# Kernel tuning notes

Hardware: AMD Instinct MI355X
Metric: run time of the kernel (lower is better)

The kernel has to match this reference:

```python
import jax, jax.numpy as jnp
import numpy as np

EMBED_DIM = 768
NUM_HEADS = 12
HEAD_DIM = EMBED_DIM // NUM_HEADS
LN_EPS = 1e-5


def setup_inputs() -> dict:
    key = jax.random.key(0)
    ks = jax.random.split(key, 10)
    D = EMBED_DIM
    s = 1.0 / np.sqrt(D)
    x = jax.random.normal(ks[0], (2, 4096, D), dtype=jnp.float32)
    # nn.Linear weights stored as [out, in]; we keep [in, out] for x @ W.
    Wq = jax.random.uniform(ks[1], (D, D), jnp.float32, -s, s)
    bq = jax.random.uniform(ks[2], (D,), jnp.float32, -s, s)
    Wk = jax.random.uniform(ks[3], (D, D), jnp.float32, -s, s)
    bk = jax.random.uniform(ks[4], (D,), jnp.float32, -s, s)
    Wv = jax.random.uniform(ks[5], (D, D), jnp.float32, -s, s)
    bv = jax.random.uniform(ks[6], (D,), jnp.float32, -s, s)
    Wo = jax.random.uniform(ks[7], (D, D), jnp.float32, -s, s)
    bo = jax.random.uniform(ks[8], (D,), jnp.float32, -s, s)
    ln_g = jnp.ones((D,), jnp.float32)
    ln_b = jnp.zeros((D,), jnp.float32)
    return {"x": x, "Wq": Wq, "bq": bq, "Wk": Wk, "bk": bk,
            "Wv": Wv, "bv": bv, "Wo": Wo, "bo": bo,
            "ln_g": ln_g, "ln_b": ln_b}


def layer_norm(x, g, b):
    mu = jnp.mean(x, axis=-1, keepdims=True)
    var = jnp.mean(jnp.square(x - mu), axis=-1, keepdims=True)
    return (x - mu) * jax.lax.rsqrt(var + LN_EPS) * g + b


def reference(x, Wq, bq, Wk, bk, Wv, bv, Wo, bo, ln_g, ln_b):
    B, S, D = x.shape
    H, Hd = NUM_HEADS, HEAD_DIM
    residual = x
    xn = layer_norm(x, ln_g, ln_b)
    # [B,S,D] -> [B,H,S,Hd]
    def heads(t):
        return t.reshape(B, S, H, Hd).transpose(0, 2, 1, 3)
    q = heads(xn @ Wq + bq)
    k = heads(xn @ Wk + bk)
    v = heads(xn @ Wv + bv)
    scores = jnp.einsum('bhqd,bhkd->bhqk', q, k) / np.sqrt(Hd).astype(np.float32)
    attn = jax.nn.softmax(scores, axis=-1)  # dropout is identity in eval
    out = jnp.einsum('bhqk,bhkd->bhqd', attn, v)
    out = out.transpose(0, 2, 1, 3).reshape(B, S, D)
    out = out @ Wo + bo
    return out + residual
```

## Files before the change

### kernel.cpp

```cpp
#include <hip/hip_runtime.h>
#include <hip/hip_bf16.h>
#include <math.h>

constexpr int Bz = 2, Sq = 4096, Dm = 768, Hn = 12, Hd = 64;
constexpr int Mrows = Bz * Sq;
constexpr int LDQKV = 2304;

typedef short bf16x8 __attribute__((ext_vector_type(8)));
typedef float f32x4 __attribute__((ext_vector_type(4)));

__device__ __forceinline__ short f2bf(float f) {
  unsigned u = __builtin_bit_cast(unsigned, f);
  u += 0x7fffu + ((u >> 16) & 1u);
  return (short)(u >> 16);
}

__device__ __forceinline__ unsigned cvt_pk_bf16(float a, float b) {
  unsigned r;
  asm("v_cvt_pk_bf16_f32 %0, %1, %2" : "=v"(r) : "v"(a), "v"(b));
  return r;
}

__global__ __launch_bounds__(256) void wprep_kernel(
    const float* __restrict__ Wq, const float* __restrict__ Wk,
    const float* __restrict__ Wv, const float* __restrict__ Wo,
    short* __restrict__ Wt) {
  __shared__ short T[64][72];
  const float* W = blockIdx.z == 0 ? Wq : blockIdx.z == 1 ? Wk
                 : blockIdx.z == 2 ? Wv : Wo;
  const int k0 = blockIdx.x * 64, n0 = blockIdx.y * 64;
  const int t = threadIdx.x;
  const int c4 = (t & 15) * 4, r = t >> 4;
#pragma unroll
  for (int i = 0; i < 4; ++i) {
    const int k = r + i * 16;
    const float4 wv = *(const float4*)(W + (size_t)(k0 + k) * 768 + n0 + c4);
    T[c4 + 0][k] = f2bf(wv.x);
    T[c4 + 1][k] = f2bf(wv.y);
    T[c4 + 2][k] = f2bf(wv.z);
    T[c4 + 3][k] = f2bf(wv.w);
  }
  __syncthreads();
  const int cn = t & 7, nn = t >> 3;
#pragma unroll
  for (int i = 0; i < 2; ++i) {
    const int n = nn + i * 32;
    *(bf16x8*)(Wt + ((size_t)blockIdx.z * 768 + n0 + n) * 768 + k0 + cn * 8) =
        *(const bf16x8*)&T[n][cn * 8];
  }
}

__global__ __launch_bounds__(256) void biaspack_kernel(
    const float* __restrict__ bq, const float* __restrict__ bk,
    const float* __restrict__ bv, const float* __restrict__ bo,
    float* __restrict__ dst) {
  const int j = blockIdx.x * 256 + threadIdx.x;
  dst[j] = j < 768 ? bq[j] : j < 1536 ? bk[j - 768]
         : j < 2304 ? bv[j - 1536] : bo[j - 2304];
}

__global__ __launch_bounds__(256) void ln_kernel(
    const float* __restrict__ x, const float* __restrict__ g,
    const float* __restrict__ b, short* __restrict__ xn) {
  const int row = blockIdx.x;
  const int t = threadIdx.x;
  const float* xr = x + (size_t)row * Dm;
  const float v0 = xr[t], v1 = xr[t + 256], v2 = xr[t + 512];
  float s = v0 + v1 + v2;
  float ss = v0 * v0 + v1 * v1 + v2 * v2;
#pragma unroll
  for (int m = 32; m >= 1; m >>= 1) {
    s += __shfl_xor(s, m);
    ss += __shfl_xor(ss, m);
  }
  __shared__ float red[8];
  const int wid = t >> 6, lane = t & 63;
  if (lane == 0) { red[wid] = s; red[4 + wid] = ss; }
  __syncthreads();
  s = red[0] + red[1] + red[2] + red[3];
  ss = red[4] + red[5] + red[6] + red[7];
  const float mu = s * (1.0f / Dm);
  const float var = ss * (1.0f / Dm) - mu * mu;
  const float rstd = rsqrtf(var + 1e-5f);
  short* xo = xn + (size_t)row * Dm;
  xo[t]       = f2bf((v0 - mu) * rstd * g[t]       + b[t]);
  xo[t + 256] = f2bf((v1 - mu) * rstd * g[t + 256] + b[t + 256]);
  xo[t + 512] = f2bf((v2 - mu) * rstd * g[t + 512] + b[t + 512]);
}

template <bool OUT_BF16, bool RESID>
__global__ __launch_bounds__(256) void gemm128_kernel(
    const short* __restrict__ A, int ldA, const short* __restrict__ Bt,
    const float* __restrict__ bias, const float* __restrict__ resid,
    void* __restrict__ C, int ldC) {
  __shared__ short As[128 * 64];
  __shared__ short Bs[128 * 64];
  const int m0 = blockIdx.x * 128, n0 = blockIdx.y * 128;
  const int t = threadIdx.x;
  const int w = t >> 6, l = t & 63;
  const int wm = w >> 1, wn = w & 1;
  const int lr = l & 15, lg = l >> 4;
  const int srow = t >> 3, sslot = t & 7;

  f32x4 acc[4][4] = {};

  for (int kt = 0; kt < 768; kt += 64) {
    bf16x8 av[4], bv[4];
#pragma unroll
    for (int it = 0; it < 4; ++it) {
      const int row = it * 32 + srow;
      av[it] = *(const bf16x8*)(A + (size_t)(m0 + row) * ldA + kt + sslot * 8);
      bv[it] = *(const bf16x8*)(Bt + (size_t)(n0 + row) * 768 + kt + sslot * 8);
    }
    __syncthreads();
#pragma unroll
    for (int it = 0; it < 4; ++it) {
      const int row = it * 32 + srow;
      const int sidx = row * 64 + ((sslot ^ (row & 7)) * 8);
      *(bf16x8*)&As[sidx] = av[it];
      *(bf16x8*)&Bs[sidx] = bv[it];
    }
    __syncthreads();
#pragma unroll
    for (int ks = 0; ks < 2; ++ks) {
      bf16x8 af[4], bfr[4];
#pragma unroll
      for (int f = 0; f < 4; ++f) {
        const int ar = wm * 64 + f * 16 + lr;
        af[f] = *(const bf16x8*)&As[ar * 64 + (((ks * 4 + lg) ^ (ar & 7)) * 8)];
        const int br = wn * 64 + f * 16 + lr;
        bfr[f] = *(const bf16x8*)&Bs[br * 64 + (((ks * 4 + lg) ^ (br & 7)) * 8)];
      }
      __builtin_amdgcn_s_setprio(1);
#pragma unroll
      for (int mf = 0; mf < 4; ++mf)
#pragma unroll
        for (int nf = 0; nf < 4; ++nf)
          acc[mf][nf] = __builtin_amdgcn_mfma_f32_16x16x32_bf16(
              af[mf], bfr[nf], acc[mf][nf], 0, 0, 0);
      __builtin_amdgcn_s_setprio(0);
    }
  }

  const int colbase = n0 + wn * 64;
  const int rowbase = m0 + wm * 64;
#pragma unroll
  for (int nf = 0; nf < 4; ++nf) {
    const int col = colbase + nf * 16 + lr;
    const float bb = bias[col];
#pragma unroll
    for (int mf = 0; mf < 4; ++mf) {
#pragma unroll
      for (int rr = 0; rr < 4; ++rr) {
        const int row = rowbase + mf * 16 + lg * 4 + rr;
        const float vv = acc[mf][nf][rr] + bb;
        if constexpr (OUT_BF16) {
          ((short*)C)[(size_t)row * ldC + col] = f2bf(vv);
        } else {
          ((float*)C)[(size_t)row * ldC + col] =
              vv + resid[(size_t)row * 768 + col];
        }
      }
    }
  }
}

__global__ __launch_bounds__(256) void vtrans_kernel(
    const short* __restrict__ vb, short* __restrict__ vt) {
  __shared__ short T[64][72];
  const int kv0 = blockIdx.x * 64;
  const int h = blockIdx.y, b = blockIdx.z;
  const int t = threadIdx.x;
  const size_t ib = ((size_t)b * Sq) * LDQKV + (size_t)h * Hd;
  const size_t ob = ((size_t)(b * Hn + h) * Hd) * Sq;
#pragma unroll
  for (int cc = 0; cc < 2; ++cc) {
    const int c = t + cc * 256;
    const int row = c >> 3, c8 = c & 7;
    const bf16x8 vv = *(const bf16x8*)(vb + ib + (size_t)(kv0 + row) * LDQKV + c8 * 8);
#pragma unroll
    for (int e = 0; e < 8; ++e) T[c8 * 8 + e][row] = vv[e];
  }
  __syncthreads();
#pragma unroll
  for (int cc = 0; cc < 2; ++cc) {
    const int c = t + cc * 256;
    const int d = c >> 3, c8 = c & 7;
    *(bf16x8*)(vt + ob + (size_t)d * Sq + kv0 + c8 * 8) = *(const bf16x8*)&T[d][c8 * 8];
  }
}

__global__ __launch_bounds__(256) void attn_mfma_kernel(
    const short* __restrict__ qg, const short* __restrict__ kg,
    const short* __restrict__ vt, short* __restrict__ o) {
  __shared__ short Ks[64 * 64];
  __shared__ short Vs[64 * 64];
  __shared__ short Ps[4][16 * 64];
  const int q0 = blockIdx.x * 64;
  const int h = blockIdx.y, b = blockIdx.z;
  const size_t qkbase = ((size_t)b * Sq) * LDQKV + (size_t)h * Hd;
  const size_t vbase = ((size_t)(b * Hn + h) * Hd) * Sq;
  const size_t obase = ((size_t)b * Sq) * Dm + (size_t)h * Hd;
  const int t = threadIdx.x;
  const int w = t >> 6, l = t & 63;
  const int lr = l & 15, lg = l >> 4;

  bf16x8 aq0, aq1;
  {
    const short* qp = qg + qkbase + (size_t)(q0 + w * 16 + lr) * LDQKV + lg * 8;
    aq0 = *(const bf16x8*)qp;
    aq1 = *(const bf16x8*)(qp + 32);
  }

  float mrow = -INFINITY;
  float lrow = 0.f;
  f32x4 oacc[4] = {};

  constexpr float SC = 0.18033688011112042f;

  const int srow = t >> 3, sslot = t & 7;
  const int srow1 = srow + 32;

  for (int kt = 0; kt < Sq; kt += 64) {
    const bf16x8 kr0 = *(const bf16x8*)(kg + qkbase + (size_t)(kt + srow) * LDQKV + sslot * 8);
    const bf16x8 kr1 = *(const bf16x8*)(kg + qkbase + (size_t)(kt + srow1) * LDQKV + sslot * 8);
    const bf16x8 vr0 = *(const bf16x8*)(vt + vbase + (size_t)srow * Sq + kt + sslot * 8);
    const bf16x8 vr1 = *(const bf16x8*)(vt + vbase + (size_t)srow1 * Sq + kt + sslot * 8);
    __syncthreads();
    *(bf16x8*)&Ks[srow * 64 + ((sslot ^ (srow & 7)) * 8)] = kr0;
    *(bf16x8*)&Ks[srow1 * 64 + ((sslot ^ (srow1 & 7)) * 8)] = kr1;
    *(bf16x8*)&Vs[srow * 64 + ((sslot ^ (srow & 7)) * 8)] = vr0;
    *(bf16x8*)&Vs[srow1 * 64 + ((sslot ^ (srow1 & 7)) * 8)] = vr1;
    __syncthreads();

    f32x4 s[4];
    __builtin_amdgcn_s_setprio(1);
#pragma unroll
    for (int nt = 0; nt < 4; ++nt) {
      const int jr = nt * 16 + lr;
      const bf16x8 k0 = *(const bf16x8*)&Ks[jr * 64 + ((lg ^ (jr & 7)) * 8)];
      const bf16x8 k1 = *(const bf16x8*)&Ks[jr * 64 + (((4 + lg) ^ (jr & 7)) * 8)];
      f32x4 acc = {};
      acc = __builtin_amdgcn_mfma_f32_16x16x32_bf16(k0, aq0, acc, 0, 0, 0);
      acc = __builtin_amdgcn_mfma_f32_16x16x32_bf16(k1, aq1, acc, 0, 0, 0);
      s[nt] = acc;
    }
    __builtin_amdgcn_s_setprio(0);

    float t0 = fmaxf(fmaxf(s[0][0], s[0][1]), fmaxf(s[0][2], s[0][3]));
    float t1 = fmaxf(fmaxf(s[1][0], s[1][1]), fmaxf(s[1][2], s[1][3]));
    float t2 = fmaxf(fmaxf(s[2][0], s[2][1]), fmaxf(s[2][2], s[2][3]));
    float t3 = fmaxf(fmaxf(s[3][0], s[3][1]), fmaxf(s[3][2], s[3][3]));
    float tm = fmaxf(fmaxf(t0, t1), fmaxf(t2, t3));
    tm = fmaxf(tm, __shfl_xor(tm, 16));
    tm = fmaxf(tm, __shfl_xor(tm, 32));
    const float mn = fmaxf(mrow, tm * SC);
    const float esc = __builtin_amdgcn_exp2f(mrow - mn);
    mrow = mn;
    const float negmn = -mn;
    float psum = 0.f;
#pragma unroll
    for (int nt = 0; nt < 4; ++nt)
#pragma unroll
      for (int r = 0; r < 4; ++r) {
        const float p = __builtin_amdgcn_exp2f(fmaf(s[nt][r], SC, negmn));
        s[nt][r] = p;
        psum += p;
      }
    lrow = lrow * esc + psum;

    float escq[4];
#pragma unroll
    for (int r = 0; r < 4; ++r) escq[r] = __shfl(esc, lg * 4 + r);
#pragma unroll
    for (int nt = 0; nt < 4; ++nt)
#pragma unroll
      for (int r = 0; r < 4; ++r) oacc[nt][r] *= escq[r];

#pragma unroll
    for (int nt = 0; nt < 4; ++nt) {
      uint2 pk;
      pk.x = cvt_pk_bf16(s[nt][0], s[nt][1]);
      pk.y = cvt_pk_bf16(s[nt][2], s[nt][3]);
      const int slot = (nt * 2 + (lg >> 1)) ^ (lr & 7);
      *(uint2*)&Ps[w][lr * 64 + slot * 8 + (lg & 1) * 4] = pk;
    }
    const bf16x8 ap0 = *(const bf16x8*)&Ps[w][lr * 64 + ((lg ^ (lr & 7)) * 8)];
    const bf16x8 ap1 = *(const bf16x8*)&Ps[w][lr * 64 + (((4 + lg) ^ (lr & 7)) * 8)];

    __builtin_amdgcn_s_setprio(1);
#pragma unroll
    for (int nt = 0; nt < 4; ++nt) {
      const int dr = nt * 16 + lr;
      const bf16x8 b0 = *(const bf16x8*)&Vs[dr * 64 + ((lg ^ (dr & 7)) * 8)];
      const bf16x8 b1 = *(const bf16x8*)&Vs[dr * 64 + (((4 + lg) ^ (dr & 7)) * 8)];
      oacc[nt] = __builtin_amdgcn_mfma_f32_16x16x32_bf16(ap0, b0, oacc[nt], 0, 0, 0);
      oacc[nt] = __builtin_amdgcn_mfma_f32_16x16x32_bf16(ap1, b1, oacc[nt], 0, 0, 0);
    }
    __builtin_amdgcn_s_setprio(0);
  }

  float lt = lrow + __shfl_xor(lrow, 16);
  lt += __shfl_xor(lt, 32);
  const float inv = 1.0f / lt;
  float invq[4];
#pragma unroll
  for (int r = 0; r < 4; ++r) invq[r] = __shfl(inv, lg * 4 + r);
#pragma unroll
  for (int r = 0; r < 4; ++r) {
    short* orow = o + obase + (size_t)(q0 + w * 16 + lg * 4 + r) * Dm;
#pragma unroll
    for (int nt = 0; nt < 4; ++nt)
      orow[nt * 16 + lr] = f2bf(oacc[nt][r] * invq[r]);
  }
}

extern "C" void kernel_launch(void* const* d_in, const int* in_sizes, int n_in,
                              void* d_out, int out_size, void* d_ws, size_t ws_size,
                              hipStream_t stream) {
  (void)in_sizes; (void)n_in; (void)out_size; (void)ws_size;
  const float* x  = (const float*)d_in[0];
  const float* Wq = (const float*)d_in[1];
  const float* bq = (const float*)d_in[2];
  const float* Wk = (const float*)d_in[3];
  const float* bk = (const float*)d_in[4];
  const float* Wv = (const float*)d_in[5];
  const float* bv = (const float*)d_in[6];
  const float* Wo = (const float*)d_in[7];
  const float* bo = (const float*)d_in[8];
  const float* lg = (const float*)d_in[9];
  const float* lb = (const float*)d_in[10];
  float* out = (float*)d_out;

  const size_t n = (size_t)Mrows * Dm;
  short* ws16 = (short*)d_ws;
  short* xn   = ws16;
  short* qkv  = xn + n;
  short* vt   = qkv + (size_t)Mrows * LDQKV;
  short* ab   = vt + n;
  short* Wt   = ab + n;
  float* ball = (float*)(Wt + (size_t)3072 * 768);

  wprep_kernel<<<dim3(12, 12, 4), 256, 0, stream>>>(Wq, Wk, Wv, Wo, Wt);
  biaspack_kernel<<<12, 256, 0, stream>>>(bq, bk, bv, bo, ball);
  ln_kernel<<<Mrows, 256, 0, stream>>>(x, lg, lb, xn);
  gemm128_kernel<true, false><<<dim3(Mrows / 128, LDQKV / 128), 256, 0, stream>>>(
      xn, Dm, Wt, ball, nullptr, qkv, LDQKV);
  vtrans_kernel<<<dim3(Sq / 64, Hn, Bz), 256, 0, stream>>>(qkv + 1536, vt);
  attn_mfma_kernel<<<dim3(Sq / 64, Hn, Bz), 256, 0, stream>>>(qkv, qkv + 768, vt, ab);
  gemm128_kernel<false, true><<<dim3(Mrows / 128, Dm / 128), 256, 0, stream>>>(
      ab, Dm, Wt + (size_t)2304 * 768, ball + 2304, x, out, Dm);
}
```

Measured before the change: 358.9 us.

## Fuse V transpose into QKV GEMM epilogue and prefetch K/V tiles in attention

The QKV GEMM epilogue now writes the V projection directly in transposed [b,h,d,s] layout using 4-element packed stores, which removes the separate vtrans kernel launch and its extra read/write of V. The attention kernel now register-prefetches the next K/V tile after the LDS stores, so global loads overlap the current tile's compute. The max reduction is also reordered. The V-path stores are narrow and strided, which may write less efficiently than the old coalesced row stores.

```diff
diff --git a/kernel.cpp b/kernel.cpp
--- a/kernel.cpp
+++ b/kernel.cpp
@@ -7,6 +7,7 @@
 constexpr int LDQKV = 2304;
 
 typedef short bf16x8 __attribute__((ext_vector_type(8)));
+typedef short s16x4 __attribute__((ext_vector_type(4)));
 typedef float f32x4 __attribute__((ext_vector_type(4)));
 
 __device__ __forceinline__ short f2bf(float f) {
@@ -88,11 +89,11 @@
   xo[t + 512] = f2bf((v2 - mu) * rstd * g[t + 512] + b[t + 512]);
 }
 
-template <bool OUT_BF16, bool RESID>
+template <bool OUT_BF16, bool RESID, bool VTFUSE>
 __global__ __launch_bounds__(256) void gemm128_kernel(
     const short* __restrict__ A, int ldA, const short* __restrict__ Bt,
     const float* __restrict__ bias, const float* __restrict__ resid,
-    void* __restrict__ C, int ldC) {
+    void* __restrict__ C, int ldC, short* __restrict__ vtp) {
   __shared__ short As[128 * 64];
   __shared__ short Bs[128 * 64];
   const int m0 = blockIdx.x * 128, n0 = blockIdx.y * 128;
@@ -144,49 +145,40 @@
 
   const int colbase = n0 + wn * 64;
   const int rowbase = m0 + wm * 64;
+  const bool vpath = VTFUSE && (n0 >= 1536);
 #pragma unroll
   for (int nf = 0; nf < 4; ++nf) {
     const int col = colbase + nf * 16 + lr;
     const float bb = bias[col];
-#pragma unroll
-    for (int mf = 0; mf < 4; ++mf) {
-#pragma unroll
-      for (int rr = 0; rr < 4; ++rr) {
-        const int row = rowbase + mf * 16 + lg * 4 + rr;
-        const float vv = acc[mf][nf][rr] + bb;
-        if constexpr (OUT_BF16) {
-          ((short*)C)[(size_t)row * ldC + col] = f2bf(vv);
-        } else {
-          ((float*)C)[(size_t)row * ldC + col] =
-              vv + resid[(size_t)row * 768 + col];
+    if (vpath) {
+      const int dcol = col - 1536;
+      const int hh = dcol >> 6, dd = dcol & 63;
+#pragma unroll
+      for (int mf = 0; mf < 4; ++mf) {
+        const int row0_ = rowbase + mf * 16 + lg * 4;
+        const int bI = row0_ >> 12;
+        const int s0 = row0_ & 4095;
+        s16x4 pk;
+#pragma unroll
+        for (int rr = 0; rr < 4; ++rr) pk[rr] = f2bf(acc[mf][nf][rr] + bb);
+        *(s16x4*)(vtp + ((size_t)(bI * Hn + hh) * Hd + dd) * Sq + s0) = pk;
+      }
+    } else {
+#pragma unroll
+      for (int mf = 0; mf < 4; ++mf) {
+#pragma unroll
+        for (int rr = 0; rr < 4; ++rr) {
+          const int row = rowbase + mf * 16 + lg * 4 + rr;
+          const float vv = acc[mf][nf][rr] + bb;
+          if constexpr (OUT_BF16) {
+            ((short*)C)[(size_t)row * ldC + col] = f2bf(vv);
+          } else {
+            ((float*)C)[(size_t)row * ldC + col] =
+                vv + resid[(size_t)row * 768 + col];
+          }
         }
       }
     }
-  }
-}
-
-__global__ __launch_bounds__(256) void vtrans_kernel(
-    const short* __restrict__ vb, short* __restrict__ vt) {
-  __shared__ short T[64][72];
-  const int kv0 = blockIdx.x * 64;
-  const int h = blockIdx.y, b = blockIdx.z;
-  const int t = threadIdx.x;
-  const size_t ib = ((size_t)b * Sq) * LDQKV + (size_t)h * Hd;
-  const size_t ob = ((size_t)(b * Hn + h) * Hd) * Sq;
-#pragma unroll
-  for (int cc = 0; cc < 2; ++cc) {
-    const int c = t + cc * 256;
-    const int row = c >> 3, c8 = c & 7;
-    const bf16x8 vv = *(const bf16x8*)(vb + ib + (size_t)(kv0 + row) * LDQKV + c8 * 8);
-#pragma unroll
-    for (int e = 0; e < 8; ++e) T[c8 * 8 + e][row] = vv[e];
-  }
-  __syncthreads();
-#pragma unroll
-  for (int cc = 0; cc < 2; ++cc) {
-    const int c = t + cc * 256;
-    const int d = c >> 3, c8 = c & 7;
-    *(bf16x8*)(vt + ob + (size_t)d * Sq + kv0 + c8 * 8) = *(const bf16x8*)&T[d][c8 * 8];
   }
 }
 
@@ -221,17 +213,26 @@
   const int srow = t >> 3, sslot = t & 7;
   const int srow1 = srow + 32;
 
+  bf16x8 kreg0 = *(const bf16x8*)(kg + qkbase + (size_t)srow * LDQKV + sslot * 8);
+  bf16x8 kreg1 = *(const bf16x8*)(kg + qkbase + (size_t)srow1 * LDQKV + sslot * 8);
+  bf16x8 vreg0 = *(const bf16x8*)(vt + vbase + (size_t)srow * Sq + sslot * 8);
+  bf16x8 vreg1 = *(const bf16x8*)(vt + vbase + (size_t)srow1 * Sq + sslot * 8);
+
   for (int kt = 0; kt < Sq; kt += 64) {
-    const bf16x8 kr0 = *(const bf16x8*)(kg + qkbase + (size_t)(kt + srow) * LDQKV + sslot * 8);
-    const bf16x8 kr1 = *(const bf16x8*)(kg + qkbase + (size_t)(kt + srow1) * LDQKV + sslot * 8);
-    const bf16x8 vr0 = *(const bf16x8*)(vt + vbase + (size_t)srow * Sq + kt + sslot * 8);
-    const bf16x8 vr1 = *(const bf16x8*)(vt + vbase + (size_t)srow1 * Sq + kt + sslot * 8);
     __syncthreads();
-    *(bf16x8*)&Ks[srow * 64 + ((sslot ^ (srow & 7)) * 8)] = kr0;
-    *(bf16x8*)&Ks[srow1 * 64 + ((sslot ^ (srow1 & 7)) * 8)] = kr1;
-    *(bf16x8*)&Vs[srow * 64 + ((sslot ^ (srow & 7)) * 8)] = vr0;
-    *(bf16x8*)&Vs[srow1 * 64 + ((sslot ^ (srow1 & 7)) * 8)] = vr1;
+    *(bf16x8*)&Ks[srow * 64 + ((sslot ^ (srow & 7)) * 8)] = kreg0;
+    *(bf16x8*)&Ks[srow1 * 64 + ((sslot ^ (srow1 & 7)) * 8)] = kreg1;
+    *(bf16x8*)&Vs[srow * 64 + ((sslot ^ (srow & 7)) * 8)] = vreg0;
+    *(bf16x8*)&Vs[srow1 * 64 + ((sslot ^ (srow1 & 7)) * 8)] = vreg1;
     __syncthreads();
+
+    if (kt + 64 < Sq) {
+      const int ktn = kt + 64;
+      kreg0 = *(const bf16x8*)(kg + qkbase + (size_t)(ktn + srow) * LDQKV + sslot * 8);
+      kreg1 = *(const bf16x8*)(kg + qkbase + (size_t)(ktn + srow1) * LDQKV + sslot * 8);
+      vreg0 = *(const bf16x8*)(vt + vbase + (size_t)srow * Sq + ktn + sslot * 8);
+      vreg1 = *(const bf16x8*)(vt + vbase + (size_t)srow1 * Sq + ktn + sslot * 8);
+    }
 
     f32x4 s[4];
     __builtin_amdgcn_s_setprio(1);
@@ -247,13 +248,15 @@
     }
     __builtin_amdgcn_s_setprio(0);
 
-    float t0 = fmaxf(fmaxf(s[0][0], s[0][1]), fmaxf(s[0][2], s[0][3]));
-    float t1 = fmaxf(fmaxf(s[1][0], s[1][1]), fmaxf(s[1][2], s[1][3]));
-    float t2 = fmaxf(fmaxf(s[2][0], s[2][1]), fmaxf(s[2][2], s[2][3]));
-    float t3 = fmaxf(fmaxf(s[3][0], s[3][1]), fmaxf(s[3][2], s[3][3]));
-    float tm = fmaxf(fmaxf(t0, t1), fmaxf(t2, t3));
+    const float a0 = fmaxf(fmaxf(s[0][0], s[0][1]), s[0][2]);
+    const float a1 = fmaxf(fmaxf(s[0][3], s[1][0]), s[1][1]);
+    const float a2 = fmaxf(fmaxf(s[1][2], s[1][3]), s[2][0]);
+    const float a3 = fmaxf(fmaxf(s[2][1], s[2][2]), s[2][3]);
+    const float a4 = fmaxf(fmaxf(s[3][0], s[3][1]), s[3][2]);
+    float tm = fmaxf(fmaxf(fmaxf(a0, a1), fmaxf(a2, a3)), fmaxf(a4, s[3][3]));
     tm = fmaxf(tm, __shfl_xor(tm, 16));
     tm = fmaxf(tm, __shfl_xor(tm, 32));
+
     const float mn = fmaxf(mrow, tm * SC);
     const float esc = __builtin_amdgcn_exp2f(mrow - mn);
     mrow = mn;
@@ -344,10 +347,9 @@
   wprep_kernel<<<dim3(12, 12, 4), 256, 0, stream>>>(Wq, Wk, Wv, Wo, Wt);
   biaspack_kernel<<<12, 256, 0, stream>>>(bq, bk, bv, bo, ball);
   ln_kernel<<<Mrows, 256, 0, stream>>>(x, lg, lb, xn);
-  gemm128_kernel<true, false><<<dim3(Mrows / 128, LDQKV / 128), 256, 0, stream>>>(
-      xn, Dm, Wt, ball, nullptr, qkv, LDQKV);
-  vtrans_kernel<<<dim3(Sq / 64, Hn, Bz), 256, 0, stream>>>(qkv + 1536, vt);
+  gemm128_kernel<true, false, true><<<dim3(Mrows / 128, LDQKV / 128), 256, 0, stream>>>(
+      xn, Dm, Wt, ball, nullptr, qkv, LDQKV, vt);
   attn_mfma_kernel<<<dim3(Sq / 64, Hn, Bz), 256, 0, stream>>>(qkv, qkv + 768, vt, ab);
-  gemm128_kernel<false, true><<<dim3(Mrows / 128, Dm / 128), 256, 0, stream>>>(
-      ab, Dm, Wt + (size_t)2304 * 768, ball + 2304, x, out, Dm);
-}
+  gemm128_kernel<false, true, false><<<dim3(Mrows / 128, Dm / 128), 256, 0, stream>>>(
+      ab, Dm, Wt + (size_t)2304 * 768, ball + 2304, x, out, Dm, nullptr);
+}
```

New measurement: 361.0 us. Within noise of the previous version (+0.6%).
